# Performance work log

Measured on AMD Instinct MI355X. Metric: run time of the kernel, lower is better.

## Reference

```python
import jax, jax.numpy as jnp
import numpy as np

N_NODES = 50000
N_RAND_EDGES = 1_600_000
IN_FEATS = 512
HIDDEN = 256
NUM_CLASSES = 64


def setup_inputs() -> dict:
    key = jax.random.key(0)
    ks = jax.random.split(key, 6)
    src = jax.random.randint(ks[0], (N_RAND_EDGES,), 0, N_NODES, dtype=jnp.int32)
    dst = jax.random.randint(ks[1], (N_RAND_EDGES,), 0, N_NODES, dtype=jnp.int32)
    # dgl.add_self_loop(g): append (i, i) for every node
    loop = jnp.arange(N_NODES, dtype=jnp.int32)
    src = jnp.concatenate([src, loop])
    dst = jnp.concatenate([dst, loop])
    features = jax.random.normal(ks[2], (N_NODES, IN_FEATS), dtype=jnp.float32)
    W_conv = jax.random.normal(ks[3], (IN_FEATS, HIDDEN), dtype=jnp.float32) * (1.0 / np.sqrt(IN_FEATS))
    b_conv = jnp.zeros((HIDDEN,), dtype=jnp.float32)
    W2 = jax.random.normal(ks[4], (HIDDEN, NUM_CLASSES), dtype=jnp.float32) * (1.0 / np.sqrt(HIDDEN))
    b2 = jnp.zeros((NUM_CLASSES,), dtype=jnp.float32)
    return {"features": features, "W_conv": W_conv, "b_conv": b_conv,
            "W2": W2, "b2": b2, "src": src, "dst": dst}


def reference(features, W_conv, b_conv, W2, b2, src, dst):
    N = features.shape[0]
    ones = jnp.ones(src.shape[0], dtype=features.dtype)
    # symmetric ('both') normalization as in DGL GraphConv; self-loops guarantee deg >= 1
    deg_out = jax.ops.segment_sum(ones, src, num_segments=N)
    deg_in = jax.ops.segment_sum(ones, dst, num_segments=N)
    norm_src = jax.lax.rsqrt(deg_out)[:, None]  # [N, 1]
    norm_dst = jax.lax.rsqrt(deg_in)[:, None]
    # in_feats > hidden -> DGL multiplies by the weight before aggregating
    h = (features @ W_conv) * norm_src            # [N, H]
    agg = jax.ops.segment_sum(h[src], dst, num_segments=N)  # sparse SpMM: gather + scatter-add
    x = jax.nn.relu(agg * norm_dst + b_conv)      # [N, H]
    # dropout: identity in eval mode (deterministic reference)
    logits = x @ W2 + b2                          # [N, C]
    return jax.nn.log_softmax(logits, axis=1)
```

## Files before the change

kernel.cpp:

```cpp
#include <hip/hip_runtime.h>

typedef unsigned char u8;
typedef unsigned short u16;
typedef unsigned int u32;
typedef __attribute__((ext_vector_type(4))) float f32x4;
typedef __attribute__((ext_vector_type(8))) short s16x8;
typedef __attribute__((ext_vector_type(4))) unsigned short u16x4;
typedef __attribute__((ext_vector_type(8))) unsigned short u16x8;

#define IN_FEATS 512
#define HIDDEN   256
#define NCLS     64
#define NB       256
#define HBINS    25000
#define EPT      7

#define H8_CLIP  2.5f
#define H8_INV   (127.0f / H8_CLIP)
#define H8_SCALE (H8_CLIP / 127.0f)

static __device__ inline u16 f2bf(float f) {
    unsigned int u = __builtin_bit_cast(unsigned int, f);
    unsigned int r = (u + 0x7FFFu + ((u >> 16) & 1u)) >> 16;
    return (u16)r;
}


__launch_bounds__(1024)
__global__ void khist(const int* __restrict__ src, const int* __restrict__ dst,
                      u16* __restrict__ P, int E, int N) {
    __shared__ u32 pk[25000];
    const int b = blockIdx.x;
    const int t = threadIdx.x;
    const int lo = (int)((long)b * E / NB);
    const int hi = (int)((long)(b + 1) * E / NB);

    int se[EPT], de[EPT];
#pragma unroll
    for (int p = 0; p < EPT; p++) {
        int e = lo + t + p * 1024;
        se[p] = 0; de[p] = 0;
        if (e < hi) { se[p] = src[e]; de[p] = dst[e]; }
    }

#pragma unroll 1
    for (int half = 0; half < 2; half++) {
        const int base = half * HBINS;
        __syncthreads();
        for (int j = t; j < 25000; j += 1024) pk[j] = 0;
        __syncthreads();
#pragma unroll
        for (int p = 0; p < EPT; p++) {
            int e = lo + t + p * 1024;
            if (e < hi) {
                unsigned rs = (unsigned)(se[p] - base), rd = (unsigned)(de[p] - base);
                if (rs < (unsigned)HBINS) atomicAdd(&pk[rs >> 1], 1u << ((rs & 1) << 4));
                if (rd < (unsigned)HBINS) atomicAdd(&pk[12500 + (rd >> 1)], 1u << ((rd & 1) << 4));
            }
        }
        for (int e = lo + t + EPT * 1024; e < hi; e += 1024) {
            int s = src[e], d = dst[e];
            unsigned rs = (unsigned)(s - base), rd = (unsigned)(d - base);
            if (rs < (unsigned)HBINS) atomicAdd(&pk[rs >> 1], 1u << ((rs & 1) << 4));
            if (rd < (unsigned)HBINS) atomicAdd(&pk[12500 + (rd >> 1)], 1u << ((rd & 1) << 4));
        }
        __syncthreads();
        for (int j = t; j < HBINS; j += 1024) {
            u32 o  = (pk[j >> 1] >> ((j & 1) << 4)) & 0xffffu;
            u32 in = (pk[12500 + (j >> 1)] >> ((j & 1) << 4)) & 0xffffu;
            P[(size_t)b * 50000 + base + j] = (u16)((o & 0xffu) | ((in & 0xffu) << 8));
        }
    }
}

__launch_bounds__(256)
__global__ void kredscan(u16* __restrict__ P, int* __restrict__ rowptr,
                         int* __restrict__ bsum, float* __restrict__ ns,
                         float* __restrict__ nd, int N) {
    __shared__ int wsum[4];
    const int b = blockIdx.x, t = threadIdx.x;
    const int lane = t & 63, wave = t >> 6;
    const int j = b * 256 + t;
    u32 si = 0;
    if (j < N) {
        u32 so = 0;
#pragma unroll 8
        for (int bb = 0; bb < NB; bb++) {
            u32 v = P[(size_t)bb * 50000 + j];
            P[(size_t)bb * 50000 + j] = (u16)si;
            so += v & 0xffu;
            si += v >> 8;
        }
        ns[j] = rsqrtf((float)so);
        nd[j] = rsqrtf((float)si);
    }
    int v = (j < N) ? (int)si : 0;
    int s = v;
#pragma unroll
    for (int off = 1; off < 64; off <<= 1) {
        int u = __shfl_up(s, off);
        if (lane >= off) s += u;
    }
    if (lane == 63) wsum[wave] = s;
    __syncthreads();
    int woff = 0;
#pragma unroll
    for (int w = 0; w < 4; w++) woff += (w < wave) ? wsum[w] : 0;
    if (j < N) rowptr[j] = woff + s - v;
    if (t == 255) bsum[b] = woff + s;
}

__launch_bounds__(256)
__global__ void kscanB(int* __restrict__ rowptr, const int* __restrict__ bsum,
                       int N, int nblk, int E) {
    __shared__ int wsum[4];
    const int b = blockIdx.x, t = threadIdx.x;
    const int lane = t & 63, wave = t >> 6;
    int v = (t < b && t < nblk) ? bsum[t] : 0;
#pragma unroll
    for (int off = 32; off; off >>= 1) v += __shfl_xor(v, off);
    if (lane == 0) wsum[wave] = v;
    __syncthreads();
    int offsum = wsum[0] + wsum[1] + wsum[2] + wsum[3];
    int j = b * 256 + t;
    if (j < N) rowptr[j] += offsum;
    if (b == 0 && t == 0) rowptr[N] = E;
}

__launch_bounds__(1024)
__global__ void kscat(const int* __restrict__ src, const int* __restrict__ dst,
                      const int* __restrict__ rowptr, const u16* __restrict__ P,
                      int* __restrict__ csc, int E, int N) {
    __shared__ int cur[HBINS];
    const int b = blockIdx.x;
    const int t = threadIdx.x;
    const int lo = (int)((long)b * E / NB);
    const int hi = (int)((long)(b + 1) * E / NB);

    int se[EPT], de[EPT];
#pragma unroll
    for (int p = 0; p < EPT; p++) {
        int e = lo + t + p * 1024;
        se[p] = 0; de[p] = 0;
        if (e < hi) { se[p] = src[e]; de[p] = dst[e]; }
    }

#pragma unroll 1
    for (int half = 0; half < 2; half++) {
        const int base = half * HBINS;
        __syncthreads();
        for (int j = t; j < HBINS; j += 1024) {
            int node = base + j;
            cur[j] = (node < N) ? rowptr[node] + (int)P[(size_t)b * 50000 + node] : 0;
        }
        __syncthreads();
#pragma unroll
        for (int p = 0; p < EPT; p++) {
            int e = lo + t + p * 1024;
            if (e < hi) {
                unsigned rd = (unsigned)(de[p] - base);
                if (rd < (unsigned)HBINS) {
                    int pos = atomicAdd(&cur[rd], 1);
                    csc[pos] = se[p] << 8;
                }
            }
        }
        for (int e = lo + t + EPT * 1024; e < hi; e += 1024) {
            int d = dst[e];
            unsigned rd = (unsigned)(d - base);
            if (rd < (unsigned)HBINS) {
                int pos = atomicAdd(&cur[rd], 1);
                csc[pos] = src[e] << 8;
            }
        }
    }
}

__global__ void kprep(const float* __restrict__ W, u16* __restrict__ Wt,
                      const float* __restrict__ W2, u16* __restrict__ W2t,
                      signed char* __restrict__ h8, int N) {
    int i = blockIdx.x * blockDim.x + threadIdx.x;
    if (i < IN_FEATS * HIDDEN) {
        int k = i >> 8, n = i & 255;
        Wt[n * IN_FEATS + k] = f2bf(W[i]);
    } else if (i < IN_FEATS * HIDDEN + HIDDEN * NCLS) {
        int ii = i - IN_FEATS * HIDDEN;
        int k = ii >> 6, n = ii & 63;
        W2t[n * HIDDEN + k] = f2bf(W2[ii]);
    } else if (i < IN_FEATS * HIDDEN + HIDDEN * NCLS + 64) {
        int ii = i - IN_FEATS * HIDDEN - HIDDEN * NCLS;
        ((int*)(h8 + (size_t)N * HIDDEN))[ii] = 0;
    }
}


static __device__ inline s16x8 ld_frag(const u16* p) {
    u16x4 lo = *(const u16x4*)p;
    u16x4 hi = *(const u16x4*)(p + 4);
    s16x8 r;
    r[0] = (short)lo.x; r[1] = (short)lo.y; r[2] = (short)lo.z; r[3] = (short)lo.w;
    r[4] = (short)hi.x; r[5] = (short)hi.y; r[6] = (short)hi.z; r[7] = (short)hi.w;
    return r;
}

__launch_bounds__(512)
__global__ void k_gemm1(const float* __restrict__ feat, const u16* __restrict__ Wt,
                        const float* __restrict__ norm_src, signed char* __restrict__ h8, int N) {
    __shared__ __align__(16) u16 At[128][40];
    __shared__ __align__(16) u16 Bt[256][40];
    const int t = threadIdx.x;
    const int lane = t & 63;
    const int wave = t >> 6;
    const int wm = wave & 1;
    const int wn = wave >> 1;
    const int m0 = blockIdx.x * 128;
    const int l15 = lane & 15;
    const int l4 = lane >> 4;

    const int r0a = t >> 3, qa = t & 7;
    const int r1a = (t + 512) >> 3;
    const int gr0 = m0 + r0a, gr1 = m0 + r1a;

    float4 pa0, pa1;
    auto LOADA = [&](int kk) {
        pa0 = (gr0 < N) ? *(const float4*)&feat[(size_t)gr0 * IN_FEATS + kk + qa * 4]
                        : make_float4(0.f, 0.f, 0.f, 0.f);
        pa1 = (gr1 < N) ? *(const float4*)&feat[(size_t)gr1 * IN_FEATS + kk + qa * 4]
                        : make_float4(0.f, 0.f, 0.f, 0.f);
    };

    f32x4 acc[4][4] = {};
    LOADA(0);

    for (int kk = 0; kk < IN_FEATS; kk += 32) {
        __syncthreads();
        {
            u16x4 p;
            p.x = f2bf(pa0.x); p.y = f2bf(pa0.y); p.z = f2bf(pa0.z); p.w = f2bf(pa0.w);
            *(u16x4*)&At[r0a][qa * 4] = p;
            p.x = f2bf(pa1.x); p.y = f2bf(pa1.y); p.z = f2bf(pa1.z); p.w = f2bf(pa1.w);
            *(u16x4*)&At[r1a][qa * 4] = p;
        }
#pragma unroll
        for (int rnd = 0; rnd < 2; rnd++) {
            int slot = t + rnd * 512;
            int r = slot >> 2, q = slot & 3;
            u16x4 w0 = *(const u16x4*)&Wt[(size_t)r * IN_FEATS + kk + q * 8];
            u16x4 w1 = *(const u16x4*)&Wt[(size_t)r * IN_FEATS + kk + q * 8 + 4];
            *(u16x4*)&Bt[r][q * 8] = w0;
            *(u16x4*)&Bt[r][q * 8 + 4] = w1;
        }
        if (kk + 32 < IN_FEATS) LOADA(kk + 32);
        __syncthreads();

        s16x8 a[4], b[4];
#pragma unroll
        for (int mi = 0; mi < 4; mi++) a[mi] = ld_frag(&At[wm * 64 + mi * 16 + l15][l4 * 8]);
#pragma unroll
        for (int ni = 0; ni < 4; ni++) b[ni] = ld_frag(&Bt[wn * 64 + ni * 16 + l15][l4 * 8]);
#pragma unroll
        for (int mi = 0; mi < 4; mi++)
#pragma unroll
            for (int ni = 0; ni < 4; ni++)
                acc[mi][ni] = __builtin_amdgcn_mfma_f32_16x16x32_bf16(a[mi], b[ni], acc[mi][ni], 0, 0, 0);
    }

#pragma unroll
    for (int mi = 0; mi < 4; mi++) {
#pragma unroll
        for (int q = 0; q < 4; q++) {
            int row = m0 + wm * 64 + mi * 16 + l4 * 4 + q;
            if (row < N) {
                float nsv = norm_src[row] * H8_INV;
#pragma unroll
                for (int ni = 0; ni < 4; ni++) {
                    int col = wn * 64 + ni * 16 + l15;
                    int v = (int)rintf(acc[mi][ni][q] * nsv);
                    v = max(-127, min(127, v));
                    h8[(size_t)row * HIDDEN + col] = (signed char)v;
                }
            }
        }
    }
}

__launch_bounds__(256)
__global__ void k_spmm(const signed char* __restrict__ h8, const int* __restrict__ rowptr,
                       const int* __restrict__ csc, const float* __restrict__ nd,
                       const float* __restrict__ bconv, u16* __restrict__ x, int N) {
    const int t = threadIdx.x;
    const int lane = t & 63;
    const int half = lane >> 5;
    const int hl = lane & 31;
    const int ZOFF = N * HIDDEN;
    const int gw = (blockIdx.x * blockDim.x + t) >> 6;
    const int nw = (gridDim.x * blockDim.x) >> 6;
    const int npair = (N + 1) >> 1;

    for (int pair = gw; pair < npair; pair += nw) {
        int node = pair * 2 + half;
        bool valid = node < N;
        int start = 0, deg = 0;
        if (valid) { start = rowptr[node]; deg = rowptr[node + 1] - start; }
        int maxdeg = max(deg, __shfl_xor(deg, 32));
        int a0 = 0, a1 = 0, a2 = 0, a3 = 0, a4 = 0, a5 = 0, a6 = 0, a7 = 0;

        for (int base = 0; base < maxdeg; base += 32) {
            int ev = ZOFF;
            if (base + hl < deg) ev = csc[start + base + hl];
            int cntmax = min(32, maxdeg - base);
            int i = 0;
            for (; i + 4 <= cntmax; i += 4) {
                int sb = (half << 5) + i;
                int o0 = __shfl(ev, sb);
                int o1 = __shfl(ev, sb + 1);
                int o2 = __shfl(ev, sb + 2);
                int o3 = __shfl(ev, sb + 3);
                int2 w0 = *(const int2*)&h8[o0 + hl * 8];
                int2 w1 = *(const int2*)&h8[o1 + hl * 8];
                int2 w2 = *(const int2*)&h8[o2 + hl * 8];
                int2 w3 = *(const int2*)&h8[o3 + hl * 8];
                a0 += ((w0.x << 24) >> 24) + ((w1.x << 24) >> 24) + ((w2.x << 24) >> 24) + ((w3.x << 24) >> 24);
                a1 += ((w0.x << 16) >> 24) + ((w1.x << 16) >> 24) + ((w2.x << 16) >> 24) + ((w3.x << 16) >> 24);
                a2 += ((w0.x << 8) >> 24) + ((w1.x << 8) >> 24) + ((w2.x << 8) >> 24) + ((w3.x << 8) >> 24);
                a3 += (w0.x >> 24) + (w1.x >> 24) + (w2.x >> 24) + (w3.x >> 24);
                a4 += ((w0.y << 24) >> 24) + ((w1.y << 24) >> 24) + ((w2.y << 24) >> 24) + ((w3.y << 24) >> 24);
                a5 += ((w0.y << 16) >> 24) + ((w1.y << 16) >> 24) + ((w2.y << 16) >> 24) + ((w3.y << 16) >> 24);
                a6 += ((w0.y << 8) >> 24) + ((w1.y << 8) >> 24) + ((w2.y << 8) >> 24) + ((w3.y << 8) >> 24);
                a7 += (w0.y >> 24) + (w1.y >> 24) + (w2.y >> 24) + (w3.y >> 24);
            }
            for (; i < cntmax; i++) {
                int o = __shfl(ev, (half << 5) + i);
                int2 w = *(const int2*)&h8[o + hl * 8];
                a0 += (w.x << 24) >> 24;
                a1 += (w.x << 16) >> 24;
                a2 += (w.x << 8) >> 24;
                a3 += w.x >> 24;
                a4 += (w.y << 24) >> 24;
                a5 += (w.y << 16) >> 24;
                a6 += (w.y << 8) >> 24;
                a7 += w.y >> 24;
            }
        }

        if (valid) {
            float scnd = nd[node] * H8_SCALE;
            float4 ba = *(const float4*)&bconv[hl * 8];
            float4 bb = *(const float4*)&bconv[hl * 8 + 4];
            u16x8 o;
            o[0] = f2bf(fmaxf((float)a0 * scnd + ba.x, 0.f));
            o[1] = f2bf(fmaxf((float)a1 * scnd + ba.y, 0.f));
            o[2] = f2bf(fmaxf((float)a2 * scnd + ba.z, 0.f));
            o[3] = f2bf(fmaxf((float)a3 * scnd + ba.w, 0.f));
            o[4] = f2bf(fmaxf((float)a4 * scnd + bb.x, 0.f));
            o[5] = f2bf(fmaxf((float)a5 * scnd + bb.y, 0.f));
            o[6] = f2bf(fmaxf((float)a6 * scnd + bb.z, 0.f));
            o[7] = f2bf(fmaxf((float)a7 * scnd + bb.w, 0.f));
            *(u16x8*)&x[(size_t)node * HIDDEN + hl * 8] = o;
        }
    }
}

__launch_bounds__(256)
__global__ void k_gemm2(const u16* __restrict__ x, const u16* __restrict__ W2t,
                        const float* __restrict__ b2, float* __restrict__ out, int N) {
    __shared__ __align__(16) u16 Bs[NCLS][HIDDEN + 8];
    const int t = threadIdx.x;
    for (int i = t; i < NCLS * HIDDEN / 8; i += 256) {
        int idx = i * 8;
        int n = idx >> 8, k = idx & 255;
        *(u16x8*)&Bs[n][k] = *(const u16x8*)&W2t[n * HIDDEN + k];
    }
    __syncthreads();

    const int lane = t & 63;
    const int wave = t >> 6;
    const int l15 = lane & 15;
    const int l4 = lane >> 4;
    const int r0 = blockIdx.x * 128 + wave * 32;

    float bb[4];
#pragma unroll
    for (int ni = 0; ni < 4; ni++) bb[ni] = b2[ni * 16 + l15];

    f32x4 acc[2][4] = {};
#pragma unroll
    for (int kk = 0; kk < HIDDEN; kk += 32) {
        s16x8 b[4];
#pragma unroll
        for (int ni = 0; ni < 4; ni++) b[ni] = ld_frag(&Bs[ni * 16 + l15][kk + l4 * 8]);
#pragma unroll
        for (int mi = 0; mi < 2; mi++) {
            int row = r0 + mi * 16 + l15;
            s16x8 a = {};
            if (row < N) a = ld_frag(&x[(size_t)row * HIDDEN + kk + l4 * 8]);
#pragma unroll
            for (int ni = 0; ni < 4; ni++)
                acc[mi][ni] = __builtin_amdgcn_mfma_f32_16x16x32_bf16(a, b[ni], acc[mi][ni], 0, 0, 0);
        }
    }

#pragma unroll
    for (int mi = 0; mi < 2; mi++) {
#pragma unroll
        for (int q = 0; q < 4; q++) {
            int row = r0 + mi * 16 + l4 * 4 + q;
            float v0 = acc[mi][0][q] + bb[0];
            float v1 = acc[mi][1][q] + bb[1];
            float v2 = acc[mi][2][q] + bb[2];
            float v3 = acc[mi][3][q] + bb[3];
            float m = fmaxf(fmaxf(v0, v1), fmaxf(v2, v3));
#pragma unroll
            for (int off = 1; off < 16; off <<= 1) m = fmaxf(m, __shfl_xor(m, off));
            float s = __expf(v0 - m) + __expf(v1 - m) + __expf(v2 - m) + __expf(v3 - m);
#pragma unroll
            for (int off = 1; off < 16; off <<= 1) s += __shfl_xor(s, off);
            float lg = m + __logf(s);
            if (row < N) {
                out[(size_t)row * NCLS + 0 * 16 + l15] = v0 - lg;
                out[(size_t)row * NCLS + 1 * 16 + l15] = v1 - lg;
                out[(size_t)row * NCLS + 2 * 16 + l15] = v2 - lg;
                out[(size_t)row * NCLS + 3 * 16 + l15] = v3 - lg;
            }
        }
    }
}


extern "C" void kernel_launch(void* const* d_in, const int* in_sizes, int n_in,
                              void* d_out, int out_size, void* d_ws, size_t ws_size,
                              hipStream_t stream) {
    const float* feat = (const float*)d_in[0];
    const float* Wc   = (const float*)d_in[1];
    const float* bc   = (const float*)d_in[2];
    const float* W2   = (const float*)d_in[3];
    const float* b2   = (const float*)d_in[4];
    const int*   src  = (const int*)d_in[5];
    const int*   dst  = (const int*)d_in[6];
    const int N = in_sizes[0] / IN_FEATS;
    const int E = in_sizes[5];
    float* out = (float*)d_out;

    char* ws = (char*)d_ws;
    size_t off = 0;
    auto alloc = [&](size_t b) {
        char* p = ws + off;
        off = (off + b + 255) & ~(size_t)255;
        return p;
    };
    signed char* h8 = (signed char*)alloc((size_t)(N + 1) * HIDDEN);
    u16* x      = (u16*)alloc((size_t)N * HIDDEN * 2);
    u16* Wt     = (u16*)alloc((size_t)IN_FEATS * HIDDEN * 2);
    u16* W2t    = (u16*)alloc((size_t)HIDDEN * NCLS * 2);
    int* rowptr = (int*)alloc((size_t)(N + 1) * 4);
    int* bsum   = (int*)alloc((size_t)256 * 4);
    float* ns   = (float*)alloc((size_t)N * 4);
    float* nd   = (float*)alloc((size_t)N * 4);
    int* csc    = (int*)alloc((size_t)E * 4);
    u16* P      = (u16*)alloc((size_t)NB * 50000 * 2);

    const int nblk = (N + 255) / 256;
    const int nprep = (IN_FEATS * HIDDEN + HIDDEN * NCLS + 64 + 255) / 256;

    khist<<<dim3(NB), dim3(1024), 0, stream>>>(src, dst, P, E, N);
    kredscan<<<dim3(nblk), dim3(256), 0, stream>>>(P, rowptr, bsum, ns, nd, N);
    kscanB<<<dim3(nblk), dim3(256), 0, stream>>>(rowptr, bsum, N, nblk, E);
    kscat<<<dim3(NB), dim3(1024), 0, stream>>>(src, dst, rowptr, P, csc, E, N);
    kprep<<<dim3(nprep), dim3(256), 0, stream>>>(Wc, Wt, W2, W2t, h8, N);
    k_gemm1<<<dim3((N + 127) / 128), dim3(512), 0, stream>>>(feat, Wt, ns, h8, N);
    k_spmm<<<dim3(2048), dim3(256), 0, stream>>>(h8, rowptr, csc, nd, bc, x, N);
    k_gemm2<<<dim3((N + 127) / 128), dim3(256), 0, stream>>>(x, W2t, b2, out, N);
}
```

Baseline: 163.2 us.

## Fuse second GEMM and log-softmax into SpMM; fold weight prep into histogram

The SpMM kernel now keeps each aggregated row in fp32 in LDS and computes the 64-class logits and log-softmax directly with scalar FMAs against a bf16 copy of W2 held in LDS. This removes the bf16 x intermediate, its global write and read, and the separate gemm2 launch. Weight transposition and h8 padding zeroing move into the first histogram kernel, which drops the kprep launch. The cost is that the small GEMM runs on vector ALUs instead of MFMA, and the SpMM blocks carry more LDS and per-node arithmetic, which may lower occupancy.

```diff
diff --git a/kernel.cpp b/kernel.cpp
--- a/kernel.cpp
+++ b/kernel.cpp
@@ -24,16 +24,37 @@
     unsigned int r = (u + 0x7FFFu + ((u >> 16) & 1u)) >> 16;
     return (u16)r;
 }
+static __device__ inline float bf2f(u16 u) {
+    unsigned int x = ((unsigned int)u) << 16;
+    return __builtin_bit_cast(float, x);
+}
 
 
 __launch_bounds__(1024)
 __global__ void khist(const int* __restrict__ src, const int* __restrict__ dst,
-                      u16* __restrict__ P, int E, int N) {
+                      u16* __restrict__ P,
+                      const float* __restrict__ W, u16* __restrict__ Wt,
+                      const float* __restrict__ W2, u16* __restrict__ W2t,
+                      signed char* __restrict__ h8, int E, int N) {
     __shared__ u32 pk[25000];
     const int b = blockIdx.x;
     const int t = threadIdx.x;
     const int lo = (int)((long)b * E / NB);
     const int hi = (int)((long)(b + 1) * E / NB);
+
+    {
+        int g = b * 1024 + t;
+        if (g < IN_FEATS * HIDDEN) {
+            int k = g >> 8, n = g & 255;
+            Wt[n * IN_FEATS + k] = f2bf(W[g]);
+        } else if (g < IN_FEATS * HIDDEN + HIDDEN * NCLS) {
+            int ii = g - IN_FEATS * HIDDEN;
+            int k = ii >> 6, n = ii & 63;
+            W2t[n * HIDDEN + k] = f2bf(W2[ii]);
+        } else if (g < IN_FEATS * HIDDEN + HIDDEN * NCLS + 64) {
+            ((int*)(h8 + (size_t)N * HIDDEN))[g - IN_FEATS * HIDDEN - HIDDEN * NCLS] = 0;
+        }
+    }
 
     int se[EPT], de[EPT];
 #pragma unroll
@@ -176,23 +197,6 @@
     }
 }
 
-__global__ void kprep(const float* __restrict__ W, u16* __restrict__ Wt,
-                      const float* __restrict__ W2, u16* __restrict__ W2t,
-                      signed char* __restrict__ h8, int N) {
-    int i = blockIdx.x * blockDim.x + threadIdx.x;
-    if (i < IN_FEATS * HIDDEN) {
-        int k = i >> 8, n = i & 255;
-        Wt[n * IN_FEATS + k] = f2bf(W[i]);
-    } else if (i < IN_FEATS * HIDDEN + HIDDEN * NCLS) {
-        int ii = i - IN_FEATS * HIDDEN;
-        int k = ii >> 6, n = ii & 63;
-        W2t[n * HIDDEN + k] = f2bf(W2[ii]);
-    } else if (i < IN_FEATS * HIDDEN + HIDDEN * NCLS + 64) {
-        int ii = i - IN_FEATS * HIDDEN - HIDDEN * NCLS;
-        ((int*)(h8 + (size_t)N * HIDDEN))[ii] = 0;
-    }
-}
-
 
 static __device__ inline s16x8 ld_frag(const u16* p) {
     u16x4 lo = *(const u16x4*)p;
@@ -287,15 +291,31 @@
 __launch_bounds__(256)
 __global__ void k_spmm(const signed char* __restrict__ h8, const int* __restrict__ rowptr,
                        const int* __restrict__ csc, const float* __restrict__ nd,
-                       const float* __restrict__ bconv, u16* __restrict__ x, int N) {
+                       const float* __restrict__ bconv, const u16* __restrict__ W2t,
+                       const float* __restrict__ b2, float* __restrict__ out, int N) {
+    __shared__ __align__(16) u16 W2s[NCLS][HIDDEN + 8];
+    __shared__ __align__(16) float xr[4][2][HIDDEN];
     const int t = threadIdx.x;
+    for (int i = t; i < NCLS * HIDDEN / 8; i += 256) {
+        int idx = i * 8;
+        int n = idx >> 8, k = idx & 255;
+        *(u16x8*)&W2s[n][k] = *(const u16x8*)&W2t[n * HIDDEN + k];
+    }
+    __syncthreads();
+
     const int lane = t & 63;
+    const int wave = t >> 6;
     const int half = lane >> 5;
     const int hl = lane & 31;
     const int ZOFF = N * HIDDEN;
     const int gw = (blockIdx.x * blockDim.x + t) >> 6;
     const int nw = (gridDim.x * blockDim.x) >> 6;
     const int npair = (N + 1) >> 1;
+
+    const float4 ba = *(const float4*)&bconv[hl * 8];
+    const float4 bb = *(const float4*)&bconv[hl * 8 + 4];
+    const float b2a = b2[hl], b2b = b2[hl + 32];
+    float* myxr = &xr[wave][half][0];
 
     for (int pair = gw; pair < npair; pair += nw) {
         int node = pair * 2 + half;
@@ -343,85 +363,44 @@
             }
         }
 
+        float scnd = nd[valid ? node : 0] * H8_SCALE;
+        float4 xv0, xv1;
+        xv0.x = fmaxf((float)a0 * scnd + ba.x, 0.f);
+        xv0.y = fmaxf((float)a1 * scnd + ba.y, 0.f);
+        xv0.z = fmaxf((float)a2 * scnd + ba.z, 0.f);
+        xv0.w = fmaxf((float)a3 * scnd + ba.w, 0.f);
+        xv1.x = fmaxf((float)a4 * scnd + bb.x, 0.f);
+        xv1.y = fmaxf((float)a5 * scnd + bb.y, 0.f);
+        xv1.z = fmaxf((float)a6 * scnd + bb.z, 0.f);
+        xv1.w = fmaxf((float)a7 * scnd + bb.w, 0.f);
+        *(float4*)&myxr[hl * 8] = xv0;
+        *(float4*)&myxr[hl * 8 + 4] = xv1;
+        asm volatile("s_waitcnt lgkmcnt(0)" ::: "memory");
+
+        float l0 = b2a, l1 = b2b;
+#pragma unroll 4
+        for (int kk = 0; kk < HIDDEN; kk += 8) {
+            float4 xa = *(const float4*)&myxr[kk];
+            float4 xb = *(const float4*)&myxr[kk + 4];
+            u16x8 w0 = *(const u16x8*)&W2s[hl][kk];
+            u16x8 w1 = *(const u16x8*)&W2s[hl + 32][kk];
+            l0 += xa.x * bf2f(w0[0]) + xa.y * bf2f(w0[1]) + xa.z * bf2f(w0[2]) + xa.w * bf2f(w0[3])
+                + xb.x * bf2f(w0[4]) + xb.y * bf2f(w0[5]) + xb.z * bf2f(w0[6]) + xb.w * bf2f(w0[7]);
+            l1 += xa.x * bf2f(w1[0]) + xa.y * bf2f(w1[1]) + xa.z * bf2f(w1[2]) + xa.w * bf2f(w1[3])
+                + xb.x * bf2f(w1[4]) + xb.y * bf2f(w1[5]) + xb.z * bf2f(w1[6]) + xb.w * bf2f(w1[7]);
+        }
+
+        float m = fmaxf(l0, l1);
+#pragma unroll
+        for (int off = 16; off; off >>= 1) m = fmaxf(m, __shfl_xor(m, off, 32));
+        float s = __expf(l0 - m) + __expf(l1 - m);
+#pragma unroll
+        for (int off = 16; off; off >>= 1) s += __shfl_xor(s, off, 32);
+        float lg = m + __logf(s);
+
         if (valid) {
-            float scnd = nd[node] * H8_SCALE;
-            float4 ba = *(const float4*)&bconv[hl * 8];
-            float4 bb = *(const float4*)&bconv[hl * 8 + 4];
-            u16x8 o;
-            o[0] = f2bf(fmaxf((float)a0 * scnd + ba.x, 0.f));
-            o[1] = f2bf(fmaxf((float)a1 * scnd + ba.y, 0.f));
-            o[2] = f2bf(fmaxf((float)a2 * scnd + ba.z, 0.f));
-            o[3] = f2bf(fmaxf((float)a3 * scnd + ba.w, 0.f));
-            o[4] = f2bf(fmaxf((float)a4 * scnd + bb.x, 0.f));
-            o[5] = f2bf(fmaxf((float)a5 * scnd + bb.y, 0.f));
-            o[6] = f2bf(fmaxf((float)a6 * scnd + bb.z, 0.f));
-            o[7] = f2bf(fmaxf((float)a7 * scnd + bb.w, 0.f));
-            *(u16x8*)&x[(size_t)node * HIDDEN + hl * 8] = o;
-        }
-    }
-}
-
-__launch_bounds__(256)
-__global__ void k_gemm2(const u16* __restrict__ x, const u16* __restrict__ W2t,
-                        const float* __restrict__ b2, float* __restrict__ out, int N) {
-    __shared__ __align__(16) u16 Bs[NCLS][HIDDEN + 8];
-    const int t = threadIdx.x;
-    for (int i = t; i < NCLS * HIDDEN / 8; i += 256) {
-        int idx = i * 8;
-        int n = idx >> 8, k = idx & 255;
-        *(u16x8*)&Bs[n][k] = *(const u16x8*)&W2t[n * HIDDEN + k];
-    }
-    __syncthreads();
-
-    const int lane = t & 63;
-    const int wave = t >> 6;
-    const int l15 = lane & 15;
-    const int l4 = lane >> 4;
-    const int r0 = blockIdx.x * 128 + wave * 32;
-
-    float bb[4];
-#pragma unroll
-    for (int ni = 0; ni < 4; ni++) bb[ni] = b2[ni * 16 + l15];
-
-    f32x4 acc[2][4] = {};
-#pragma unroll
-    for (int kk = 0; kk < HIDDEN; kk += 32) {
-        s16x8 b[4];
-#pragma unroll
-        for (int ni = 0; ni < 4; ni++) b[ni] = ld_frag(&Bs[ni * 16 + l15][kk + l4 * 8]);
-#pragma unroll
-        for (int mi = 0; mi < 2; mi++) {
-            int row = r0 + mi * 16 + l15;
-            s16x8 a = {};
-            if (row < N) a = ld_frag(&x[(size_t)row * HIDDEN + kk + l4 * 8]);
-#pragma unroll
-            for (int ni = 0; ni < 4; ni++)
-                acc[mi][ni] = __builtin_amdgcn_mfma_f32_16x16x32_bf16(a, b[ni], acc[mi][ni], 0, 0, 0);
-        }
-    }
-
-#pragma unroll
-    for (int mi = 0; mi < 2; mi++) {
-#pragma unroll
-        for (int q = 0; q < 4; q++) {
-            int row = r0 + mi * 16 + l4 * 4 + q;
-            float v0 = acc[mi][0][q] + bb[0];
-            float v1 = acc[mi][1][q] + bb[1];
-            float v2 = acc[mi][2][q] + bb[2];
-            float v3 = acc[mi][3][q] + bb[3];
-            float m = fmaxf(fmaxf(v0, v1), fmaxf(v2, v3));
-#pragma unroll
-            for (int off = 1; off < 16; off <<= 1) m = fmaxf(m, __shfl_xor(m, off));
-            float s = __expf(v0 - m) + __expf(v1 - m) + __expf(v2 - m) + __expf(v3 - m);
-#pragma unroll
-            for (int off = 1; off < 16; off <<= 1) s += __shfl_xor(s, off);
-            float lg = m + __logf(s);
-            if (row < N) {
-                out[(size_t)row * NCLS + 0 * 16 + l15] = v0 - lg;
-                out[(size_t)row * NCLS + 1 * 16 + l15] = v1 - lg;
-                out[(size_t)row * NCLS + 2 * 16 + l15] = v2 - lg;
-                out[(size_t)row * NCLS + 3 * 16 + l15] = v3 - lg;
-            }
+            out[(size_t)node * NCLS + hl] = l0 - lg;
+            out[(size_t)node * NCLS + 32 + hl] = l1 - lg;
         }
     }
 }
@@ -449,7 +428,6 @@
         return p;
     };
     signed char* h8 = (signed char*)alloc((size_t)(N + 1) * HIDDEN);
-    u16* x      = (u16*)alloc((size_t)N * HIDDEN * 2);
     u16* Wt     = (u16*)alloc((size_t)IN_FEATS * HIDDEN * 2);
     u16* W2t    = (u16*)alloc((size_t)HIDDEN * NCLS * 2);
     int* rowptr = (int*)alloc((size_t)(N + 1) * 4);
@@ -460,14 +438,11 @@
     u16* P      = (u16*)alloc((size_t)NB * 50000 * 2);
 
     const int nblk = (N + 255) / 256;
-    const int nprep = (IN_FEATS * HIDDEN + HIDDEN * NCLS + 64 + 255) / 256;
-
-    khist<<<dim3(NB), dim3(1024), 0, stream>>>(src, dst, P, E, N);
+
+    khist<<<dim3(NB), dim3(1024), 0, stream>>>(src, dst, P, Wc, Wt, W2, W2t, h8, E, N);
     kredscan<<<dim3(nblk), dim3(256), 0, stream>>>(P, rowptr, bsum, ns, nd, N);
     kscanB<<<dim3(nblk), dim3(256), 0, stream>>>(rowptr, bsum, N, nblk, E);
     kscat<<<dim3(NB), dim3(1024), 0, stream>>>(src, dst, rowptr, P, csc, E, N);
-    kprep<<<dim3(nprep), dim3(256), 0, stream>>>(Wc, Wt, W2, W2t, h8, N);
     k_gemm1<<<dim3((N + 127) / 128), dim3(512), 0, stream>>>(feat, Wt, ns, h8, N);
-    k_spmm<<<dim3(2048), dim3(256), 0, stream>>>(h8, rowptr, csc, nd, bc, x, N);
-    k_gemm2<<<dim3((N + 127) / 128), dim3(256), 0, stream>>>(x, W2t, b2, out, N);
-}
+    k_spmm<<<dim3(2048), dim3(256), 0, stream>>>(h8, rowptr, csc, nd, bc, W2t, b2, out, N);
+}
```

After: 202.6 us. +24.2%, slower.
